# Optimization experiments

Hardware: AMD Instinct MI355X
Metric: run time of the kernel (lower is better)

The kernel has to match this reference:

```python
import jax, jax.numpy as jnp
import numpy as np
import math

B, S, D = 4, 1024, 512
H, DK, DV = 8, 64, 64
NEG = -1.0e9
LN_EPS = 1e-5


def setup_inputs() -> dict:
    key = jax.random.key(0)
    ks = jax.random.split(key, 12)
    sc = 1.0 / math.sqrt(D)
    inp = {
        "input_Q": jax.random.normal(ks[0], (B, S, D), jnp.float32),
        "input_K": jax.random.normal(ks[1], (B, S, D), jnp.float32),
        "input_V": jax.random.normal(ks[2], (B, S, D), jnp.float32),
        "attn_mask": jax.random.randint(ks[3], (B, S, S), 0, 2).astype(bool),
        "bias_mask": jax.random.randint(ks[4], (B, S, S), 0, 2).astype(bool),
        "Wq": jax.random.normal(ks[5], (D, H * DK), jnp.float32) * sc,
        "Wk": jax.random.normal(ks[6], (D, H * DK), jnp.float32) * sc,
        "Wq2": jax.random.normal(ks[7], (D, H * DK), jnp.float32) * sc,
        "Wk2": jax.random.normal(ks[8], (D, H * DK), jnp.float32) * sc,
        "Wv": jax.random.normal(ks[9], (D, H * DV), jnp.float32) * sc,
        "Wo": jax.random.normal(ks[10], (H * DV, D), jnp.float32) * sc,
        "ln_g": jnp.ones((D,), jnp.float32),
        "ln_b": jnp.zeros((D,), jnp.float32),
    }
    return inp


def _heads(x, W, d):
    b, s, _ = x.shape
    return (x @ W).reshape(b, s, H, d).transpose(0, 2, 1, 3)  # [B,H,S,d]


def reference(input_Q, input_K, input_V, attn_mask, bias_mask,
              Wq, Wk, Wq2, Wk2, Wv, Wo, ln_g, ln_b):
    residual = input_Q
    Q = _heads(input_Q, Wq, DK)
    K = _heads(input_K, Wk, DK)
    V = _heads(input_V, Wv, DV)
    Q2 = _heads(input_Q, Wq2, DK)
    K2 = _heads(input_K, Wk2, DK)

    am = attn_mask[:, None, :, :]   # broadcast over heads
    bm = bias_mask[:, None, :, :]

    scores1 = jnp.einsum('bhqd,bhkd->bhqk', Q, K) / math.sqrt(DK)
    bias = jnp.einsum('bhqd,bhkd->bhqk', Q2, K2)
    bias = jnp.where(bm, NEG, bias)
    scores = jnp.where(am, NEG, scores1 + bias)
    attn = jax.nn.softmax(scores, axis=-1)          # [B,H,S,S]
    context = jnp.einsum('bhqk,bhkd->bhqd', attn, V)  # [B,H,S,DV]
    context = context.transpose(0, 2, 1, 3).reshape(B, S, H * DV)
    output = context @ Wo

    x = output + residual
    mu = jnp.mean(x, axis=-1, keepdims=True)
    var = jnp.mean(jnp.square(x - mu), axis=-1, keepdims=True)
    out = (x - mu) / jnp.sqrt(var + LN_EPS) * ln_g + ln_b
    return (out, attn)
```

## Files before the change

kernel.cpp:

```cpp
#include <hip/hip_runtime.h>
#include <hip/hip_fp16.h>

typedef _Float16 f16x8 __attribute__((ext_vector_type(8)));
typedef _Float16 f16x4 __attribute__((ext_vector_type(4)));
typedef float f32x4 __attribute__((ext_vector_type(4)));

__global__ __launch_bounds__(256) void wtrans6_kernel(
    const float* __restrict__ Wq, const float* __restrict__ Wk,
    const float* __restrict__ Wq2, const float* __restrict__ Wk2,
    const float* __restrict__ Wv, const float* __restrict__ Wo,
    __half* __restrict__ WqcT, __half* __restrict__ WkcT,
    __half* __restrict__ WvT, __half* __restrict__ WoT) {
  const float* src;
  __half* dst;
  float scale = 1.0f;
  switch (blockIdx.z) {
    case 0: src = Wq;  dst = WqcT;              scale = 0.125f; break;
    case 1: src = Wq2; dst = WqcT + 512 * 512;  break;
    case 2: src = Wk;  dst = WkcT;              break;
    case 3: src = Wk2; dst = WkcT + 512 * 512;  break;
    case 4: src = Wv;  dst = WvT;               break;
    default: src = Wo; dst = WoT;               break;
  }
  __shared__ float t[32][33];
  int n0 = blockIdx.x * 32, k0 = blockIdx.y * 32;
  int tx = threadIdx.x, ty = threadIdx.y;
#pragma unroll
  for (int i = 0; i < 4; i++)
    t[ty + i * 8][tx] = src[(size_t)(k0 + ty + i * 8) * 512 + n0 + tx];
  __syncthreads();
#pragma unroll
  for (int i = 0; i < 4; i++)
    dst[(size_t)(n0 + ty + i * 8) * 512 + k0 + tx] = __float2half(t[tx][ty + i * 8] * scale);
}

__device__ __forceinline__ void maskprep_body(const int* __restrict__ am,
                                              const int* __restrict__ bm,
                                              uint32_t* __restrict__ packed, int bk,
                                              int t) {
  int w = bk & 3, bqt = bk >> 2, qt = bqt & 31, b = bqt >> 5;
  int mi = t >> 6, lane = t & 63;
  int lg = lane >> 4, l15 = lane & 15;
  int qbase = qt * 32 + mi * 16 + lg * 4;
  int kbase = w * 256 + l15;
  uint32_t outw[4] = {0u, 0u, 0u, 0u};
#pragma unroll
  for (int kt = 0; kt < 16; kt++) {
    int k = kbase + kt * 16;
#pragma unroll
    for (int r = 0; r < 4; r++) {
      size_t idx = ((size_t)(b * 1024 + qbase + r)) * 1024 + k;
      uint32_t code = (am[idx] ? 1u : 0u) + (bm[idx] ? 1u : 0u);
      outw[kt >> 2] |= code << (((kt & 3) << 3) + (r << 1));
    }
  }
  uint4* dst = (uint4*)packed + ((size_t)bk * 64 + lane) * 2 + mi;
  *dst = make_uint4(outw[0], outw[1], outw[2], outw[3]);
}

template <int AF32, int MODE>
__device__ __forceinline__ void gemm_body(const void* Ap, const __half* Bt, __half* C,
                                          int N, int bx, int by,
                                          __half* __restrict__ pk) {
  __shared__ __align__(16) _Float16 smem[10240];
  _Float16(*As)[40] = (_Float16(*)[40])smem;
  _Float16(*Bs)[40] = (_Float16(*)[40])(smem + 5120);
  int tid = threadIdx.x;
  int wave = tid >> 6, lane = tid & 63;
  int lg = lane >> 4, l15 = lane & 15;
  int wm = (wave >> 1) * 64, wn = (wave & 1) * 64;
  int bm0 = by * 128, bn0 = bx * 128;
  int srow = tid >> 1, sseg = (tid & 1) * 16;
  const float* Af = (const float*)Ap;
  const __half* Ah = (const __half*)Ap;
  f32x4 acc[4][4];
#pragma unroll
  for (int i = 0; i < 4; i++)
#pragma unroll
    for (int j = 0; j < 4; j++) acc[i][j] = (f32x4){0.f, 0.f, 0.f, 0.f};

  for (int kt = 0; kt < 16; kt++) {
    int k0 = kt * 32;
    if (AF32) {
      const float* s = Af + (size_t)(bm0 + srow) * 512 + k0 + sseg;
      _Float16* d = &As[srow][sseg];
#pragma unroll
      for (int i = 0; i < 16; i += 4) {
        float4 v = *(const float4*)(s + i);
        d[i] = (_Float16)v.x; d[i + 1] = (_Float16)v.y;
        d[i + 2] = (_Float16)v.z; d[i + 3] = (_Float16)v.w;
      }
    } else {
      const __half* s = Ah + (size_t)(bm0 + srow) * 512 + k0 + sseg;
      *(uint4*)&As[srow][sseg] = *(const uint4*)s;
      *(uint4*)(&As[srow][sseg] + 8) = *(const uint4*)(s + 8);
    }
    {
      const __half* s = Bt + (size_t)(bn0 + srow) * 512 + k0 + sseg;
      *(uint4*)&Bs[srow][sseg] = *(const uint4*)s;
      *(uint4*)(&Bs[srow][sseg] + 8) = *(const uint4*)(s + 8);
    }
    __syncthreads();
    f16x8 af[4], bf[4];
#pragma unroll
    for (int i = 0; i < 4; i++) af[i] = *(const f16x8*)&As[wm + i * 16 + l15][lg * 8];
#pragma unroll
    for (int j = 0; j < 4; j++) bf[j] = *(const f16x8*)&Bs[wn + j * 16 + l15][lg * 8];
#pragma unroll
    for (int i = 0; i < 4; i++)
#pragma unroll
      for (int j = 0; j < 4; j++)
        acc[i][j] = __builtin_amdgcn_mfma_f32_16x16x32_f16(af[i], bf[j], acc[i][j], 0, 0, 0);
    __syncthreads();
  }

  _Float16* cb = smem;
#pragma unroll
  for (int ph = 0; ph < 2; ph++) {
    __syncthreads();
    if ((wave >> 1) == ph) {
#pragma unroll
      for (int i = 0; i < 4; i++)
#pragma unroll
        for (int j = 0; j < 4; j++)
#pragma unroll
          for (int r = 0; r < 4; r++)
            cb[(i * 16 + lg * 4 + r) * 136 + wn + j * 16 + l15] =
                (_Float16)acc[i][j][r];
    }
    __syncthreads();
    if (MODE == 0) {
#pragma unroll
      for (int rr = 0; rr < 4; rr++) {
        int row = rr * 16 + (tid >> 4);
        int colh = (tid & 15) * 8;
        uint4 v = *(const uint4*)&cb[row * 136 + colh];
        *(uint4*)&C[(size_t)(bm0 + ph * 64 + row) * N + bn0 + colh] = v;
      }
    } else if (MODE == 2) {
      int m0 = bm0 + ph * 64;
      int b = m0 >> 10;
      int kblk0 = (m0 & 1023) >> 4;
      int isK2 = (bn0 >= 512) ? 1 : 0;
      int hpair = (isK2 ? (bx - 4) : bx) * 2;
      int sel = tid >> 6;
      int hh = sel >> 1, ksl = sel & 1;
      int bh = b * 8 + hpair + hh;
      int ksd = isK2 * 2 + ksl;
#pragma unroll
      for (int kb = 0; kb < 4; kb++) {
        f16x8 v = *(const f16x8*)&cb[(kb * 16 + l15) * 136 + hh * 64 + ksl * 32 + lg * 8];
        *(f16x8*)(pk + ((((size_t)bh * 64 + kblk0 + kb) * 4 + ksd) * 64 + lane) * 8) = v;
      }
    } else {
      int m0 = bm0 + ph * 64;
      int b = m0 >> 10;
      int k320 = (m0 & 1023) >> 5;
      int sel = tid >> 6;
      int hh = sel >> 1, kk2 = sel & 1;
      int bh = b * 8 + bx * 2 + hh;
#pragma unroll
      for (int dvb = 0; dvb < 4; dvb++) {
        f16x8 v;
#pragma unroll
        for (int j = 0; j < 8; j++)
          v[j] = cb[(kk2 * 32 + lg * 8 + j) * 136 + hh * 64 + dvb * 16 + l15];
        *(f16x8*)(pk + ((((size_t)bh * 32 + k320 + kk2) * 4 + dvb) * 64 + lane) * 8) = v;
      }
    }
  }
}

__global__ __launch_bounds__(256) void proj_kernel(
    const float* __restrict__ inQ, const float* __restrict__ inK,
    const float* __restrict__ inV, const __half* __restrict__ WqcT,
    const __half* __restrict__ WkcT, const __half* __restrict__ WvT,
    const int* __restrict__ am, const int* __restrict__ bm,
    __half* __restrict__ QQ2, __half* __restrict__ Kpk, __half* __restrict__ Vpk,
    uint32_t* __restrict__ packed) {
  int z = blockIdx.z;
  if (z == 0) {
    gemm_body<1, 0>(inQ, WqcT, QQ2, 1024, blockIdx.x, blockIdx.y, nullptr);
  } else if (z == 1) {
    gemm_body<1, 2>(inK, WkcT, nullptr, 1024, blockIdx.x, blockIdx.y, Kpk);
  } else if (z == 2) {
    if (blockIdx.x >= 4) return;
    gemm_body<1, 1>(inV, WvT, nullptr, 512, blockIdx.x, blockIdx.y, Vpk);
  } else {
    int bk = (blockIdx.y * 8 + blockIdx.x) * 2 + (threadIdx.x >> 7);
    maskprep_body(am, bm, packed, bk, threadIdx.x & 127);
  }
}

__global__ __launch_bounds__(256) void gemm_f16_kernel(const __half* __restrict__ A,
                                                       const __half* __restrict__ Bt,
                                                       __half* __restrict__ C, int N) {
  gemm_body<0, 0>(A, Bt, C, N, blockIdx.x, blockIdx.y, nullptr);
}

__global__ __launch_bounds__(256, 2) void attn_kernel(
    const __half* __restrict__ QQ2, const __half* __restrict__ Kpk,
    const __half* __restrict__ Vpk, const uint32_t* __restrict__ packed,
    float* __restrict__ attn_out, __half* __restrict__ CTX) {
  int qt = blockIdx.x, bh = blockIdx.y;
  int b = bh >> 3, h = bh & 7;
  int q0 = qt * 32;
  int tid = threadIdx.x;
  int wave = tid >> 6, lane = tid & 63;
  int lg = lane >> 4, l15 = lane & 15;
  int kw = wave * 256;

  __shared__ __align__(16) _Float16 P[4][32][264];
  __shared__ float redmax[4][32], redsum[4][32];

  f16x8 qf[2][4];
  const __half* Qb = QQ2 + ((size_t)(b * 1024 + q0)) * 1024 + h * 64;
#pragma unroll
  for (int mi = 0; mi < 2; mi++)
#pragma unroll
    for (int ks = 0; ks < 4; ks++) {
      int off = (ks < 2) ? ks * 32 : 512 + (ks - 2) * 32;
      qf[mi][ks] = *(const f16x8*)(Qb + (size_t)(mi * 16 + l15) * 1024 + off + lg * 8);
    }

  uint4 mw[2];
  {
    const uint4* mp =
        (const uint4*)packed + ((size_t)((b * 32 + qt) * 4 + wave) * 64 + lane) * 2;
    mw[0] = mp[0];
    mw[1] = mp[1];
  }

  f16x4 sc16[2][16];
  float mx[2][4];
#pragma unroll
  for (int mi = 0; mi < 2; mi++)
#pragma unroll
    for (int r = 0; r < 4; r++) mx[mi][r] = -3.0e38f;
  const __half* Kbp = Kpk + ((size_t)bh * 64 + wave * 16) * 4 * 512 + lane * 8;
#pragma unroll
  for (int kt = 0; kt < 16; kt++) {
    const __half* kp = Kbp + (size_t)kt * 4 * 512;
    f16x8 kf[4];
    kf[0] = *(const f16x8*)kp;
    kf[1] = *(const f16x8*)(kp + 512);
    kf[2] = *(const f16x8*)(kp + 1024);
    kf[3] = *(const f16x8*)(kp + 1536);
#pragma unroll
    for (int mi = 0; mi < 2; mi++) {
      f32x4 s = (f32x4){0.f, 0.f, 0.f, 0.f};
#pragma unroll
      for (int ks = 0; ks < 4; ks++)
        s = __builtin_amdgcn_mfma_f32_16x16x32_f16(qf[mi][ks], kf[ks], s, 0, 0, 0);
      uint32_t mword = ((const uint32_t*)&mw[mi])[kt >> 2];
      f16x4 sv;
#pragma unroll
      for (int r = 0; r < 4; r++) {
        uint32_t code = (mword >> (((kt & 3) << 3) + (r << 1))) & 3u;
        float sval = s[r] - 30000.0f * (float)code;
        sv[r] = (_Float16)sval;
        mx[mi][r] = fmaxf(mx[mi][r], (float)sv[r]);
      }
      sc16[mi][kt] = sv;
    }
  }

#pragma unroll
  for (int mi = 0; mi < 2; mi++)
#pragma unroll
    for (int r = 0; r < 4; r++) {
      float m = mx[mi][r];
#pragma unroll
      for (int o = 1; o < 16; o <<= 1) m = fmaxf(m, __shfl_xor(m, o));
      if (l15 == 0) redmax[wave][mi * 16 + lg * 4 + r] = m;
    }
  __syncthreads();
  float mfin[2][4];
#pragma unroll
  for (int mi = 0; mi < 2; mi++)
#pragma unroll
    for (int r = 0; r < 4; r++) {
      int row = mi * 16 + lg * 4 + r;
      mfin[mi][r] = fmaxf(fmaxf(redmax[0][row], redmax[1][row]),
                          fmaxf(redmax[2][row], redmax[3][row]));
    }

  float sm[2][4];
#pragma unroll
  for (int mi = 0; mi < 2; mi++)
#pragma unroll
    for (int r = 0; r < 4; r++) sm[mi][r] = 0.f;
#pragma unroll
  for (int kt = 0; kt < 16; kt++)
#pragma unroll
    for (int mi = 0; mi < 2; mi++) {
      f16x4 sv = sc16[mi][kt];
      f16x4 pv;
#pragma unroll
      for (int r = 0; r < 4; r++) {
        float p = __expf((float)sv[r] - mfin[mi][r]);
        sm[mi][r] += p;
        pv[r] = (_Float16)p;
      }
      sc16[mi][kt] = pv;
    }
#pragma unroll
  for (int mi = 0; mi < 2; mi++)
#pragma unroll
    for (int r = 0; r < 4; r++) {
      float s = sm[mi][r];
#pragma unroll
      for (int o = 1; o < 16; o <<= 1) s += __shfl_xor(s, o);
      if (l15 == 0) redsum[wave][mi * 16 + lg * 4 + r] = s;
    }
  __syncthreads();
  float inv[2][4];
#pragma unroll
  for (int mi = 0; mi < 2; mi++)
#pragma unroll
    for (int r = 0; r < 4; r++) {
      int row = mi * 16 + lg * 4 + r;
      inv[mi][r] =
          1.0f / (redsum[0][row] + redsum[1][row] + redsum[2][row] + redsum[3][row]);
    }

  float* ab = attn_out + ((size_t)bh * 1024 + q0) * 1024;
#pragma unroll
  for (int mi = 0; mi < 2; mi++)
#pragma unroll
    for (int kt = 0; kt < 16; kt++)
#pragma unroll
      for (int r = 0; r < 4; r++) {
        int row = mi * 16 + lg * 4 + r;
        int col = kw + kt * 16 + l15;
        float a = (float)sc16[mi][kt][r] * inv[mi][r];
        ab[(size_t)row * 1024 + col] = a;
        P[wave][row][kt * 16 + l15] = (_Float16)a;
      }
  __syncthreads();

  f32x4 ctx[2];
  ctx[0] = (f32x4){0.f, 0.f, 0.f, 0.f};
  ctx[1] = (f32x4){0.f, 0.f, 0.f, 0.f};
  const __half* Vbp = Vpk + ((size_t)bh * 32 * 4 + wave) * 512 + lane * 8;
#pragma unroll
  for (int c = 0; c < 4; c++) {
#pragma unroll
    for (int kk = 0; kk < 8; kk++) {
      int k32 = c * 8 + kk;
      f16x8 pa0 = *(const f16x8*)&P[c][l15][kk * 32 + lg * 8];
      f16x8 pa1 = *(const f16x8*)&P[c][16 + l15][kk * 32 + lg * 8];
      f16x8 vf = *(const f16x8*)(Vbp + (size_t)k32 * 4 * 512);
      ctx[0] = __builtin_amdgcn_mfma_f32_16x16x32_f16(pa0, vf, ctx[0], 0, 0, 0);
      ctx[1] = __builtin_amdgcn_mfma_f32_16x16x32_f16(pa1, vf, ctx[1], 0, 0, 0);
    }
  }

#pragma unroll
  for (int mi = 0; mi < 2; mi++)
#pragma unroll
    for (int r = 0; r < 4; r++) {
      int row = mi * 16 + lg * 4 + r;
      CTX[(size_t)(b * 1024 + q0 + row) * 512 + h * 64 + wave * 16 + l15] =
          __float2half(ctx[mi][r]);
    }
}

__global__ __launch_bounds__(256) void ln_kernel(const __half* __restrict__ O,
                                                 const float* __restrict__ resid,
                                                 const float* __restrict__ g,
                                                 const float* __restrict__ bb,
                                                 float* __restrict__ out) {
  int w = threadIdx.x >> 6, lane = threadIdx.x & 63;
  int row = blockIdx.x * 4 + w;
  size_t base = (size_t)row * 512 + lane * 8;
  f16x8 ov = *(const f16x8*)(O + base);
  float4 r0 = *(const float4*)(resid + base);
  float4 r1 = *(const float4*)(resid + base + 4);
  float x[8];
  x[0] = (float)ov[0] + r0.x; x[1] = (float)ov[1] + r0.y;
  x[2] = (float)ov[2] + r0.z; x[3] = (float)ov[3] + r0.w;
  x[4] = (float)ov[4] + r1.x; x[5] = (float)ov[5] + r1.y;
  x[6] = (float)ov[6] + r1.z; x[7] = (float)ov[7] + r1.w;
  float s = 0.f;
#pragma unroll
  for (int i = 0; i < 8; i++) s += x[i];
#pragma unroll
  for (int o = 1; o < 64; o <<= 1) s += __shfl_xor(s, o);
  float mean = s * (1.0f / 512.0f);
  float d[8], v = 0.f;
#pragma unroll
  for (int i = 0; i < 8; i++) { d[i] = x[i] - mean; v += d[i] * d[i]; }
#pragma unroll
  for (int o = 1; o < 64; o <<= 1) v += __shfl_xor(v, o);
  float rs = rsqrtf(v * (1.0f / 512.0f) + 1e-5f);
  float4 g0 = *(const float4*)(g + lane * 8);
  float4 g1 = *(const float4*)(g + lane * 8 + 4);
  float4 b0 = *(const float4*)(bb + lane * 8);
  float4 b1 = *(const float4*)(bb + lane * 8 + 4);
  f32x4 o0 = {d[0] * rs * g0.x + b0.x, d[1] * rs * g0.y + b0.y,
              d[2] * rs * g0.z + b0.z, d[3] * rs * g0.w + b0.w};
  f32x4 o1 = {d[4] * rs * g1.x + b1.x, d[5] * rs * g1.y + b1.y,
              d[6] * rs * g1.z + b1.z, d[7] * rs * g1.w + b1.w};
  __builtin_nontemporal_store(o0, (f32x4*)(out + base));
  __builtin_nontemporal_store(o1, (f32x4*)(out + base + 4));
}

extern "C" void kernel_launch(void* const* d_in, const int* in_sizes, int n_in,
                              void* d_out, int out_size, void* d_ws, size_t ws_size,
                              hipStream_t stream) {
  const float* inQ = (const float*)d_in[0];
  const float* inK = (const float*)d_in[1];
  const float* inV = (const float*)d_in[2];
  const int* am = (const int*)d_in[3];
  const int* bmk = (const int*)d_in[4];
  const float* Wq = (const float*)d_in[5];
  const float* Wk = (const float*)d_in[6];
  const float* Wq2 = (const float*)d_in[7];
  const float* Wk2 = (const float*)d_in[8];
  const float* Wv = (const float*)d_in[9];
  const float* Wo = (const float*)d_in[10];
  const float* lng = (const float*)d_in[11];
  const float* lnb = (const float*)d_in[12];

  char* ws = (char*)d_ws;
  __half* WqcT = (__half*)ws; ws += (size_t)1024 * 512 * 2;
  __half* WkcT = (__half*)ws; ws += (size_t)1024 * 512 * 2;
  __half* WvT = (__half*)ws;  ws += (size_t)512 * 512 * 2;
  __half* WoT = (__half*)ws;  ws += (size_t)512 * 512 * 2;
  __half* QQ2 = (__half*)ws;  ws += (size_t)4096 * 1024 * 2;
  __half* Kpk = (__half*)ws;  ws += (size_t)4096 * 1024 * 2;
  __half* Vpk = (__half*)ws;  ws += (size_t)4096 * 512 * 2;
  __half* CTX = (__half*)ws;  ws += (size_t)4096 * 512 * 2;
  __half* Obuf = (__half*)ws; ws += (size_t)4096 * 512 * 2;
  uint32_t* packed = (uint32_t*)Obuf;

  float* out0 = (float*)d_out;
  float* attn_out = out0 + (size_t)4 * 1024 * 512;

  wtrans6_kernel<<<dim3(16, 16, 6), dim3(32, 8), 0, stream>>>(Wq, Wk, Wq2, Wk2, Wv, Wo,
                                                              WqcT, WkcT, WvT, WoT);
  proj_kernel<<<dim3(8, 32, 4), 256, 0, stream>>>(inQ, inK, inV, WqcT, WkcT, WvT, am,
                                                  bmk, QQ2, Kpk, Vpk, packed);
  attn_kernel<<<dim3(32, 32), 256, 0, stream>>>(QQ2, Kpk, Vpk, packed, attn_out, CTX);
  gemm_f16_kernel<<<dim3(4, 32), 256, 0, stream>>>(CTX, WoT, Obuf, 512);
  ln_kernel<<<1024, 256, 0, stream>>>(Obuf, inQ, lng, lnb, out0);
}
```

Baseline: 127.6 us.

## Split attention key range across eight waves with cross-wave context reduction

The attention kernel now runs 512 threads (8 waves) per block, each wave covering 128 keys instead of 256. The softmax reductions are widened to 8 partials and P is stored as a shared 32x1024 tile. The P·V step is split across two key halves and four value-dim blocks, with the halves combined through shared memory. Mask packing is rearranged to match the 128-key-per-wave layout. The aim is fewer registers per wave and more waves in flight, at the cost of more shared memory and an extra barrier and reduction.

```diff
diff --git a/kernel.cpp b/kernel.cpp
--- a/kernel.cpp
+++ b/kernel.cpp
@@ -38,14 +38,14 @@
                                               const int* __restrict__ bm,
                                               uint32_t* __restrict__ packed, int bk,
                                               int t) {
-  int w = bk & 3, bqt = bk >> 2, qt = bqt & 31, b = bqt >> 5;
+  int w = bk & 7, bqt = bk >> 3, qt = bqt & 31, b = bqt >> 5;
   int mi = t >> 6, lane = t & 63;
   int lg = lane >> 4, l15 = lane & 15;
   int qbase = qt * 32 + mi * 16 + lg * 4;
-  int kbase = w * 256 + l15;
-  uint32_t outw[4] = {0u, 0u, 0u, 0u};
-#pragma unroll
-  for (int kt = 0; kt < 16; kt++) {
+  int kbase = w * 128 + l15;
+  uint32_t outw[2] = {0u, 0u};
+#pragma unroll
+  for (int kt = 0; kt < 8; kt++) {
     int k = kbase + kt * 16;
 #pragma unroll
     for (int r = 0; r < 4; r++) {
@@ -54,8 +54,8 @@
       outw[kt >> 2] |= code << (((kt & 3) << 3) + (r << 1));
     }
   }
-  uint4* dst = (uint4*)packed + ((size_t)bk * 64 + lane) * 2 + mi;
-  *dst = make_uint4(outw[0], outw[1], outw[2], outw[3]);
+  uint2* dst = (uint2*)packed + ((size_t)bk * 64 + lane) * 2 + mi;
+  *dst = make_uint2(outw[0], outw[1]);
 }
 
 template <int AF32, int MODE>
@@ -187,8 +187,11 @@
     if (blockIdx.x >= 4) return;
     gemm_body<1, 1>(inV, WvT, nullptr, 512, blockIdx.x, blockIdx.y, Vpk);
   } else {
-    int bk = (blockIdx.y * 8 + blockIdx.x) * 2 + (threadIdx.x >> 7);
-    maskprep_body(am, bm, packed, bk, threadIdx.x & 127);
+    int base = (blockIdx.y * 8 + blockIdx.x) * 4;
+    int sub = threadIdx.x >> 7;
+    int t = threadIdx.x & 127;
+    maskprep_body(am, bm, packed, base + sub, t);
+    maskprep_body(am, bm, packed, base + 2 + sub, t);
   }
 }
 
@@ -198,7 +201,7 @@
   gemm_body<0, 0>(A, Bt, C, N, blockIdx.x, blockIdx.y, nullptr);
 }
 
-__global__ __launch_bounds__(256, 2) void attn_kernel(
+__global__ __launch_bounds__(512, 4) void attn_kernel(
     const __half* __restrict__ QQ2, const __half* __restrict__ Kpk,
     const __half* __restrict__ Vpk, const uint32_t* __restrict__ packed,
     float* __restrict__ attn_out, __half* __restrict__ CTX) {
@@ -208,10 +211,11 @@
   int tid = threadIdx.x;
   int wave = tid >> 6, lane = tid & 63;
   int lg = lane >> 4, l15 = lane & 15;
-  int kw = wave * 256;
-
-  __shared__ __align__(16) _Float16 P[4][32][264];
-  __shared__ float redmax[4][32], redsum[4][32];
+  int kw = wave * 128;
+
+  __shared__ __align__(16) _Float16 P[32][1032];
+  __shared__ float redmax[8][32], redsum[8][32];
+  __shared__ float cred[32][66];
 
   f16x8 qf[2][4];
   const __half* Qb = QQ2 + ((size_t)(b * 1024 + q0)) * 1024 + h * 64;
@@ -223,23 +227,23 @@
       qf[mi][ks] = *(const f16x8*)(Qb + (size_t)(mi * 16 + l15) * 1024 + off + lg * 8);
     }
 
-  uint4 mw[2];
+  uint2 mw[2];
   {
-    const uint4* mp =
-        (const uint4*)packed + ((size_t)((b * 32 + qt) * 4 + wave) * 64 + lane) * 2;
+    const uint2* mp =
+        (const uint2*)packed + ((size_t)((b * 32 + qt) * 8 + wave) * 64 + lane) * 2;
     mw[0] = mp[0];
     mw[1] = mp[1];
   }
 
-  f16x4 sc16[2][16];
+  f16x4 sc16[2][8];
   float mx[2][4];
 #pragma unroll
   for (int mi = 0; mi < 2; mi++)
 #pragma unroll
     for (int r = 0; r < 4; r++) mx[mi][r] = -3.0e38f;
-  const __half* Kbp = Kpk + ((size_t)bh * 64 + wave * 16) * 4 * 512 + lane * 8;
-#pragma unroll
-  for (int kt = 0; kt < 16; kt++) {
+  const __half* Kbp = Kpk + ((size_t)(bh * 64 + wave * 8)) * 4 * 512 + lane * 8;
+#pragma unroll
+  for (int kt = 0; kt < 8; kt++) {
     const __half* kp = Kbp + (size_t)kt * 4 * 512;
     f16x8 kf[4];
     kf[0] = *(const f16x8*)kp;
@@ -252,7 +256,7 @@
 #pragma unroll
       for (int ks = 0; ks < 4; ks++)
         s = __builtin_amdgcn_mfma_f32_16x16x32_f16(qf[mi][ks], kf[ks], s, 0, 0, 0);
-      uint32_t mword = ((const uint32_t*)&mw[mi])[kt >> 2];
+      uint32_t mword = (kt < 4) ? mw[mi].x : mw[mi].y;
       f16x4 sv;
 #pragma unroll
       for (int r = 0; r < 4; r++) {
@@ -281,8 +285,11 @@
 #pragma unroll
     for (int r = 0; r < 4; r++) {
       int row = mi * 16 + lg * 4 + r;
-      mfin[mi][r] = fmaxf(fmaxf(redmax[0][row], redmax[1][row]),
-                          fmaxf(redmax[2][row], redmax[3][row]));
+      float m0 = fmaxf(fmaxf(redmax[0][row], redmax[1][row]),
+                       fmaxf(redmax[2][row], redmax[3][row]));
+      float m1 = fmaxf(fmaxf(redmax[4][row], redmax[5][row]),
+                       fmaxf(redmax[6][row], redmax[7][row]));
+      mfin[mi][r] = fmaxf(m0, m1);
     }
 
   float sm[2][4];
@@ -291,7 +298,7 @@
 #pragma unroll
     for (int r = 0; r < 4; r++) sm[mi][r] = 0.f;
 #pragma unroll
-  for (int kt = 0; kt < 16; kt++)
+  for (int kt = 0; kt < 8; kt++)
 #pragma unroll
     for (int mi = 0; mi < 2; mi++) {
       f16x4 sv = sc16[mi][kt];
@@ -320,50 +327,61 @@
 #pragma unroll
     for (int r = 0; r < 4; r++) {
       int row = mi * 16 + lg * 4 + r;
-      inv[mi][r] =
-          1.0f / (redsum[0][row] + redsum[1][row] + redsum[2][row] + redsum[3][row]);
+      inv[mi][r] = 1.0f / (redsum[0][row] + redsum[1][row] + redsum[2][row] +
+                           redsum[3][row] + redsum[4][row] + redsum[5][row] +
+                           redsum[6][row] + redsum[7][row]);
     }
 
   float* ab = attn_out + ((size_t)bh * 1024 + q0) * 1024;
 #pragma unroll
   for (int mi = 0; mi < 2; mi++)
 #pragma unroll
-    for (int kt = 0; kt < 16; kt++)
+    for (int kt = 0; kt < 8; kt++)
 #pragma unroll
       for (int r = 0; r < 4; r++) {
         int row = mi * 16 + lg * 4 + r;
         int col = kw + kt * 16 + l15;
         float a = (float)sc16[mi][kt][r] * inv[mi][r];
         ab[(size_t)row * 1024 + col] = a;
-        P[wave][row][kt * 16 + l15] = (_Float16)a;
+        P[row][col] = (_Float16)a;
       }
   __syncthreads();
 
+  int kh = wave >> 2;
+  int dvb = wave & 3;
   f32x4 ctx[2];
   ctx[0] = (f32x4){0.f, 0.f, 0.f, 0.f};
   ctx[1] = (f32x4){0.f, 0.f, 0.f, 0.f};
-  const __half* Vbp = Vpk + ((size_t)bh * 32 * 4 + wave) * 512 + lane * 8;
-#pragma unroll
-  for (int c = 0; c < 4; c++) {
-#pragma unroll
-    for (int kk = 0; kk < 8; kk++) {
-      int k32 = c * 8 + kk;
-      f16x8 pa0 = *(const f16x8*)&P[c][l15][kk * 32 + lg * 8];
-      f16x8 pa1 = *(const f16x8*)&P[c][16 + l15][kk * 32 + lg * 8];
-      f16x8 vf = *(const f16x8*)(Vbp + (size_t)k32 * 4 * 512);
-      ctx[0] = __builtin_amdgcn_mfma_f32_16x16x32_f16(pa0, vf, ctx[0], 0, 0, 0);
-      ctx[1] = __builtin_amdgcn_mfma_f32_16x16x32_f16(pa1, vf, ctx[1], 0, 0, 0);
-    }
-  }
-
-#pragma unroll
-  for (int mi = 0; mi < 2; mi++)
-#pragma unroll
-    for (int r = 0; r < 4; r++) {
-      int row = mi * 16 + lg * 4 + r;
-      CTX[(size_t)(b * 1024 + q0 + row) * 512 + h * 64 + wave * 16 + l15] =
-          __float2half(ctx[mi][r]);
-    }
+  const _Float16* Pb = &P[0][kh * 512];
+#pragma unroll
+  for (int kk = 0; kk < 16; kk++) {
+    int k32 = kh * 16 + kk;
+    f16x8 pa0 = *(const f16x8*)(Pb + (size_t)l15 * 1032 + kk * 32 + lg * 8);
+    f16x8 pa1 = *(const f16x8*)(Pb + (size_t)(16 + l15) * 1032 + kk * 32 + lg * 8);
+    f16x8 vf = *(const f16x8*)(Vpk +
+                               (((size_t)(bh * 32 + k32) * 4 + dvb) * 64 + lane) * 8);
+    ctx[0] = __builtin_amdgcn_mfma_f32_16x16x32_f16(pa0, vf, ctx[0], 0, 0, 0);
+    ctx[1] = __builtin_amdgcn_mfma_f32_16x16x32_f16(pa1, vf, ctx[1], 0, 0, 0);
+  }
+  if (kh == 1) {
+#pragma unroll
+    for (int mi = 0; mi < 2; mi++)
+#pragma unroll
+      for (int r = 0; r < 4; r++)
+        cred[mi * 16 + lg * 4 + r][dvb * 16 + l15] = ctx[mi][r];
+  }
+  __syncthreads();
+  if (kh == 0) {
+#pragma unroll
+    for (int mi = 0; mi < 2; mi++)
+#pragma unroll
+      for (int r = 0; r < 4; r++) {
+        int row = mi * 16 + lg * 4 + r;
+        float v = ctx[mi][r] + cred[row][dvb * 16 + l15];
+        CTX[(size_t)(b * 1024 + q0 + row) * 512 + h * 64 + dvb * 16 + l15] =
+            __float2half(v);
+      }
+  }
 }
 
 __global__ __launch_bounds__(256) void ln_kernel(const __half* __restrict__ O,
@@ -442,7 +460,7 @@
                                                               WqcT, WkcT, WvT, WoT);
   proj_kernel<<<dim3(8, 32, 4), 256, 0, stream>>>(inQ, inK, inV, WqcT, WkcT, WvT, am,
                                                   bmk, QQ2, Kpk, Vpk, packed);
-  attn_kernel<<<dim3(32, 32), 256, 0, stream>>>(QQ2, Kpk, Vpk, packed, attn_out, CTX);
+  attn_kernel<<<dim3(32, 32), 512, 0, stream>>>(QQ2, Kpk, Vpk, packed, attn_out, CTX);
   gemm_f16_kernel<<<dim3(4, 32), 256, 0, stream>>>(CTX, WoT, Obuf, 512);
   ln_kernel<<<1024, 256, 0, stream>>>(Obuf, inQ, lng, lnb, out0);
 }
```

New measurement: 132.8 us. 1.04x slower.

## Fuse output projection GEMM with residual add and LayerNorm

Applied to the files above, without the earlier changes.

Replaces the separate Wo GEMM and LayerNorm kernels with one kernel. Each 512-thread block computes a 64-row by full-512-column output tile with MFMA, stages it in shared memory, then applies the residual add and LayerNorm before writing the result. This removes one launch and the round trip of the intermediate output through global memory. The cost is a grid of only 64 blocks, far fewer than the GPU has compute units, so the GEMM phase may be underutilized. It also has no double buffering, a 512x32 B tile loaded per k-step, and about 65 KB of shared memory per block.

```diff
diff --git a/kernel.cpp b/kernel.cpp
--- a/kernel.cpp
+++ b/kernel.cpp
@@ -192,12 +192,6 @@
   }
 }
 
-__global__ __launch_bounds__(256) void gemm_f16_kernel(const __half* __restrict__ A,
-                                                       const __half* __restrict__ Bt,
-                                                       __half* __restrict__ C, int N) {
-  gemm_body<0, 0>(A, Bt, C, N, blockIdx.x, blockIdx.y, nullptr);
-}
-
 __global__ __launch_bounds__(256, 2) void attn_kernel(
     const __half* __restrict__ QQ2, const __half* __restrict__ Kpk,
     const __half* __restrict__ Vpk, const uint32_t* __restrict__ packed,
@@ -366,44 +360,97 @@
     }
 }
 
-__global__ __launch_bounds__(256) void ln_kernel(const __half* __restrict__ O,
-                                                 const float* __restrict__ resid,
-                                                 const float* __restrict__ g,
-                                                 const float* __restrict__ bb,
-                                                 float* __restrict__ out) {
-  int w = threadIdx.x >> 6, lane = threadIdx.x & 63;
-  int row = blockIdx.x * 4 + w;
-  size_t base = (size_t)row * 512 + lane * 8;
-  f16x8 ov = *(const f16x8*)(O + base);
-  float4 r0 = *(const float4*)(resid + base);
-  float4 r1 = *(const float4*)(resid + base + 4);
-  float x[8];
-  x[0] = (float)ov[0] + r0.x; x[1] = (float)ov[1] + r0.y;
-  x[2] = (float)ov[2] + r0.z; x[3] = (float)ov[3] + r0.w;
-  x[4] = (float)ov[4] + r1.x; x[5] = (float)ov[5] + r1.y;
-  x[6] = (float)ov[6] + r1.z; x[7] = (float)ov[7] + r1.w;
-  float s = 0.f;
-#pragma unroll
-  for (int i = 0; i < 8; i++) s += x[i];
-#pragma unroll
-  for (int o = 1; o < 64; o <<= 1) s += __shfl_xor(s, o);
-  float mean = s * (1.0f / 512.0f);
-  float d[8], v = 0.f;
-#pragma unroll
-  for (int i = 0; i < 8; i++) { d[i] = x[i] - mean; v += d[i] * d[i]; }
-#pragma unroll
-  for (int o = 1; o < 64; o <<= 1) v += __shfl_xor(v, o);
-  float rs = rsqrtf(v * (1.0f / 512.0f) + 1e-5f);
+__global__ __launch_bounds__(512) void woln_kernel(
+    const __half* __restrict__ CTX, const __half* __restrict__ WoT,
+    const float* __restrict__ resid, const float* __restrict__ g,
+    const float* __restrict__ bb, float* __restrict__ out) {
+  __shared__ __align__(16) char smemraw[66560];
+  _Float16(*As)[40] = (_Float16(*)[40])smemraw;
+  _Float16(*Bs)[40] = (_Float16(*)[40])(smemraw + 5120);
+  int tid = threadIdx.x;
+  int wave = tid >> 6, lane = tid & 63;
+  int lg = lane >> 4, l15 = lane & 15;
+  int bm0 = blockIdx.x * 64;
+  int wn = wave * 64;
+  f32x4 acc[4][4];
+#pragma unroll
+  for (int i = 0; i < 4; i++)
+#pragma unroll
+    for (int j = 0; j < 4; j++) acc[i][j] = (f32x4){0.f, 0.f, 0.f, 0.f};
+
+  for (int kt = 0; kt < 16; kt++) {
+    int k0 = kt * 32;
+    {
+      int row = tid >> 3, off = (tid & 7) * 4;
+      *(uint2*)&As[row][off] =
+          *(const uint2*)(CTX + (size_t)(bm0 + row) * 512 + k0 + off);
+    }
+    {
+      const __half* s = WoT + (size_t)tid * 512 + k0;
+      *(uint4*)&Bs[tid][0] = *(const uint4*)s;
+      *(uint4*)&Bs[tid][8] = *(const uint4*)(s + 8);
+      *(uint4*)&Bs[tid][16] = *(const uint4*)(s + 16);
+      *(uint4*)&Bs[tid][24] = *(const uint4*)(s + 24);
+    }
+    __syncthreads();
+    f16x8 af[4], bf[4];
+#pragma unroll
+    for (int i = 0; i < 4; i++) af[i] = *(const f16x8*)&As[i * 16 + l15][lg * 8];
+#pragma unroll
+    for (int j = 0; j < 4; j++) bf[j] = *(const f16x8*)&Bs[wn + j * 16 + l15][lg * 8];
+#pragma unroll
+    for (int i = 0; i < 4; i++)
+#pragma unroll
+      for (int j = 0; j < 4; j++)
+        acc[i][j] = __builtin_amdgcn_mfma_f32_16x16x32_f16(af[i], bf[j], acc[i][j], 0, 0, 0);
+    __syncthreads();
+  }
+
+  _Float16(*cb)[520] = (_Float16(*)[520])smemraw;
+#pragma unroll
+  for (int i = 0; i < 4; i++)
+#pragma unroll
+    for (int j = 0; j < 4; j++)
+#pragma unroll
+      for (int r = 0; r < 4; r++)
+        cb[i * 16 + lg * 4 + r][wn + j * 16 + l15] = (_Float16)acc[i][j][r];
+  __syncthreads();
+
   float4 g0 = *(const float4*)(g + lane * 8);
   float4 g1 = *(const float4*)(g + lane * 8 + 4);
   float4 b0 = *(const float4*)(bb + lane * 8);
   float4 b1 = *(const float4*)(bb + lane * 8 + 4);
-  f32x4 o0 = {d[0] * rs * g0.x + b0.x, d[1] * rs * g0.y + b0.y,
-              d[2] * rs * g0.z + b0.z, d[3] * rs * g0.w + b0.w};
-  f32x4 o1 = {d[4] * rs * g1.x + b1.x, d[5] * rs * g1.y + b1.y,
-              d[6] * rs * g1.z + b1.z, d[7] * rs * g1.w + b1.w};
-  __builtin_nontemporal_store(o0, (f32x4*)(out + base));
-  __builtin_nontemporal_store(o1, (f32x4*)(out + base + 4));
+#pragma unroll
+  for (int rr = 0; rr < 8; rr++) {
+    int row = wave * 8 + rr;
+    size_t base = (size_t)(bm0 + row) * 512 + lane * 8;
+    f16x8 ov = *(const f16x8*)&cb[row][lane * 8];
+    float4 r0 = *(const float4*)(resid + base);
+    float4 r1 = *(const float4*)(resid + base + 4);
+    float x[8];
+    x[0] = (float)ov[0] + r0.x; x[1] = (float)ov[1] + r0.y;
+    x[2] = (float)ov[2] + r0.z; x[3] = (float)ov[3] + r0.w;
+    x[4] = (float)ov[4] + r1.x; x[5] = (float)ov[5] + r1.y;
+    x[6] = (float)ov[6] + r1.z; x[7] = (float)ov[7] + r1.w;
+    float s = 0.f;
+#pragma unroll
+    for (int i = 0; i < 8; i++) s += x[i];
+#pragma unroll
+    for (int o = 1; o < 64; o <<= 1) s += __shfl_xor(s, o);
+    float mean = s * (1.0f / 512.0f);
+    float d[8], v = 0.f;
+#pragma unroll
+    for (int i = 0; i < 8; i++) { d[i] = x[i] - mean; v += d[i] * d[i]; }
+#pragma unroll
+    for (int o = 1; o < 64; o <<= 1) v += __shfl_xor(v, o);
+    float rs = rsqrtf(v * (1.0f / 512.0f) + 1e-5f);
+    f32x4 o0 = {d[0] * rs * g0.x + b0.x, d[1] * rs * g0.y + b0.y,
+                d[2] * rs * g0.z + b0.z, d[3] * rs * g0.w + b0.w};
+    f32x4 o1 = {d[4] * rs * g1.x + b1.x, d[5] * rs * g1.y + b1.y,
+                d[6] * rs * g1.z + b1.z, d[7] * rs * g1.w + b1.w};
+    __builtin_nontemporal_store(o0, (f32x4*)(out + base));
+    __builtin_nontemporal_store(o1, (f32x4*)(out + base + 4));
+  }
 }
 
 extern "C" void kernel_launch(void* const* d_in, const int* in_sizes, int n_in,
@@ -432,8 +479,7 @@
   __half* Kpk = (__half*)ws;  ws += (size_t)4096 * 1024 * 2;
   __half* Vpk = (__half*)ws;  ws += (size_t)4096 * 512 * 2;
   __half* CTX = (__half*)ws;  ws += (size_t)4096 * 512 * 2;
-  __half* Obuf = (__half*)ws; ws += (size_t)4096 * 512 * 2;
-  uint32_t* packed = (uint32_t*)Obuf;
+  uint32_t* packed = (uint32_t*)ws; ws += (size_t)512 * 64 * 2 * 16;
 
   float* out0 = (float*)d_out;
   float* attn_out = out0 + (size_t)4 * 1024 * 512;
@@ -443,6 +489,5 @@
   proj_kernel<<<dim3(8, 32, 4), 256, 0, stream>>>(inQ, inK, inV, WqcT, WkcT, WvT, am,
                                                   bmk, QQ2, Kpk, Vpk, packed);
   attn_kernel<<<dim3(32, 32), 256, 0, stream>>>(QQ2, Kpk, Vpk, packed, attn_out, CTX);
-  gemm_f16_kernel<<<dim3(4, 32), 256, 0, stream>>>(CTX, WoT, Obuf, 512);
-  ln_kernel<<<1024, 256, 0, stream>>>(Obuf, inQ, lng, lnb, out0);
-}
+  woln_kernel<<<64, 512, 0, stream>>>(CTX, WoT, inQ, lng, lnb, out0);
+}
```

After: 145.1 us. 13.7% more time.
